# Kernel optimization log

Hardware: AMD Instinct MI355X
Metric: run time of the kernel (lower is better)

## Reference

```python
import jax, jax.numpy as jnp
import numpy as np

B, T, D, H, d = 2, 2048, 1024, 16, 64
INNER = H * d
SCALE = d ** -0.5


def _rope(x, inv_freq):
    # x: [B, H, T, d], interleaved rotary as in the torch module
    t = x.shape[2]
    pos = jnp.arange(t, dtype=jnp.float32)
    freqs = pos[:, None] * inv_freq[None, :]          # [T, d/2]
    cos_f, sin_f = jnp.cos(freqs), jnp.sin(freqs)
    x1, x2 = x[..., 0::2], x[..., 1::2]
    y1 = x1 * cos_f - x2 * sin_f
    y2 = x1 * sin_f + x2 * cos_f
    return jnp.stack([y1, y2], axis=-1).reshape(x.shape)


def setup_inputs() -> dict:
    key = jax.random.key(0)
    ks = jax.random.split(key, 6)
    x = jax.random.normal(ks[0], (B, T, D), jnp.float32)
    W_qkv = jax.random.normal(ks[1], (D, 3 * INNER), jnp.float32) * (D ** -0.5)
    W_out = jax.random.normal(ks[2], (INNER, D), jnp.float32) * (INNER ** -0.5)
    W_dt = jax.random.normal(ks[3], (D, H), jnp.float32) * 0.01
    b_dt = jnp.full((H,), -4.0, jnp.float32)
    W_gsp = jax.random.normal(ks[4], (D, INNER), jnp.float32) * 0.01
    b_gsp = jnp.full((INNER,), -3.0, jnp.float32)
    inv_freq = 1.0 / (10000.0 ** (jnp.arange(0, d, 2, dtype=jnp.float32) / d))
    return {"x": x, "W_qkv": W_qkv, "W_out": W_out, "W_dt": W_dt,
            "b_dt": b_dt, "W_gsp": W_gsp, "b_gsp": b_gsp, "inv_freq": inv_freq}


def reference(x, W_qkv, W_out, W_dt, b_dt, W_gsp, b_gsp, inv_freq):
    qkv = (x @ W_qkv).reshape(B, T, 3, H, d)
    Q = jnp.moveaxis(qkv[:, :, 0], 1, 2)   # [B,H,T,d]
    K = jnp.moveaxis(qkv[:, :, 1], 1, 2)
    V = jnp.moveaxis(qkv[:, :, 2], 1, 2)
    Q = _rope(Q, inv_freq)
    K = _rope(K, inv_freq)

    dt = jax.nn.softplus(x @ W_dt + b_dt)             # [B,T,H]
    gamma = jnp.moveaxis(jnp.exp(-dt), 1, 2)          # [B,H,T]

    p = jax.nn.sigmoid(x @ W_gsp + b_gsp).reshape(B, T, H, d)
    p = jnp.moveaxis(p, 1, 2)                          # [B,H,T,d]
    gamma_eff = gamma[..., None] * (1.0 - p) + p
    gamma_scalar = gamma_eff.mean(axis=-1)            # [B,H,T]
    V = V * (1.0 - p)

    log_gamma = jnp.log(jnp.clip(gamma_scalar, 1e-6, 1.0 - 1e-6))
    lgc = jnp.cumsum(log_gamma, axis=-1)              # [B,H,T]
    log_D = jnp.clip(lgc[..., :, None] - lgc[..., None, :], -20.0, 0.0)
    causal = jnp.tril(jnp.ones((T, T), jnp.float32))
    Dm = jnp.exp(log_D) * causal                      # [B,H,T,T]

    Wscore = jnp.einsum('bhtd,bhsd->bhts', Q * SCALE, K)
    A = Wscore * Dm
    Y = jnp.einsum('bhts,bhsd->bhtd', A, V)
    Y = jnp.moveaxis(Y, 1, 2).reshape(B, T, INNER)
    return Y @ W_out
```

## Files before the change

### kernel.cpp

```cpp
#include <hip/hip_runtime.h>
#include <hip/hip_bf16.h>
#include <math.h>

#define B_     2
#define T_     2048
#define D_     1024
#define H_     16
#define INNER_ 1024
#define NC_    4096
#define SCALE_ 0.125f

typedef unsigned short u16;
typedef short short8 __attribute__((ext_vector_type(8)));
typedef float f32x4 __attribute__((ext_vector_type(4)));
typedef float f32x16 __attribute__((ext_vector_type(16)));
typedef unsigned short u16x4 __attribute__((ext_vector_type(4)));
typedef unsigned int u32x2 __attribute__((ext_vector_type(2)));

__device__ __forceinline__ u16 f2bf(float x) {
  union { float f; unsigned u; } v; v.f = x;
  unsigned r = v.u + 0x7fffu + ((v.u >> 16) & 1u);
  return (u16)(r >> 16);
}
__device__ __forceinline__ float b2f(u16 x) {
  union { unsigned u; float f; } v; v.u = ((unsigned)x) << 16;
  return v.f;
}
__device__ __forceinline__ unsigned cvtpk(float lo, float hi) {
  unsigned r;
  asm("v_cvt_pk_bf16_f32 %0, %1, %2" : "=v"(r) : "v"(lo), "v"(hi));
  return r;
}
__device__ __forceinline__ void gload16(const void* g, void* l) {
  __builtin_amdgcn_global_load_lds(
      (const __attribute__((address_space(1))) void*)g,
      (__attribute__((address_space(3))) void*)l, 16, 0, 0);
}

__global__ __launch_bounds__(256) void prep_kernel(
    const float* __restrict__ x, const float* __restrict__ W_qkv,
    const float* __restrict__ W_gsp, const float* __restrict__ W_out,
    const float* __restrict__ W_dt, const float* __restrict__ inv_freq,
    u16* __restrict__ xb, u16* __restrict__ Wcombt, u16* __restrict__ Woutt,
    u16* __restrict__ Wdtb, float2* __restrict__ tab) {
  const int bid = blockIdx.x, tid = threadIdx.x;
  if (bid < 1280) {
    const float* src; u16* dst; int N, nx, ky;
    if (bid < 768)       { src = W_qkv; dst = Wcombt;                N = 3072; nx = bid % 48;          ky = bid / 48; }
    else if (bid < 1024) { src = W_gsp; dst = Wcombt + 3072 * 1024;  N = 1024; nx = (bid - 768) % 16;  ky = (bid - 768) / 16; }
    else                 { src = W_out; dst = Woutt;                 N = 1024; nx = (bid - 1024) % 16; ky = (bid - 1024) / 16; }
    __shared__ float tile[64][65];
    const int k0 = ky * 64, n0 = nx * 64;
    for (int e = tid; e < 4096; e += 256) {
      int kk = e >> 6, nn = e & 63;
      tile[kk][nn] = src[(size_t)(k0 + kk) * N + n0 + nn];
    }
    __syncthreads();
    for (int e = tid; e < 4096; e += 256) {
      int nn = e >> 6, kk = e & 63;
      dst[(size_t)(n0 + nn) * 1024 + k0 + kk] = f2bf(tile[kk][nn]);
    }
  } else if (bid < 1344) {
    int i = (bid - 1280) * 256 + tid;
    int k = i >> 4, h = i & 15;
    Wdtb[(size_t)h * D_ + k] = f2bf(W_dt[i]);
  } else if (bid < 1600) {
    int i = (bid - 1344) * 256 + tid;
    int t = i >> 5, j = i & 31;
    float s, c;
    sincosf((float)t * inv_freq[j], &s, &c);
    tab[i] = make_float2(c, s);
  } else {
    int base = (bid - 1600) * 1024 + tid;
#pragma unroll
    for (int r = 0; r < 4; ++r) {
      int i = base + r * 256;
      float4 v = *reinterpret_cast<const float4*>(x + (size_t)i * 4);
      u16x4 o; o.x = f2bf(v.x); o.y = f2bf(v.y); o.z = f2bf(v.z); o.w = f2bf(v.w);
      *reinterpret_cast<u16x4*>(xb + (size_t)i * 4) = o;
    }
  }
}

__global__ __launch_bounds__(256) void gamma_kernel(
    const u16* __restrict__ xb, const u16* __restrict__ Wdtb,
    const float* __restrict__ b_dt, float* __restrict__ gam) {
  const int row = blockIdx.x * 4 + (threadIdx.x >> 6);
  const int l = threadIdx.x & 63;
  const int h = l >> 2;
  const int kc = (l & 3) * 256;
  const short8* xp = (const short8*)(xb + (size_t)row * D_ + kc);
  const short8* wp = (const short8*)(Wdtb + h * D_ + kc);
  float s = 0.f;
#pragma unroll
  for (int i = 0; i < 32; ++i) {
    short8 xv = xp[i], wv = wp[i];
#pragma unroll
    for (int j = 0; j < 8; ++j) s += b2f((u16)xv[j]) * b2f((u16)wv[j]);
  }
  s += __shfl_xor(s, 1);
  s += __shfl_xor(s, 2);
  if ((l & 3) == 0) {
    float v = s + b_dt[h];
    float sp = (v > 20.f) ? v : log1pf(__expf(v));
    gam[row * H_ + h] = __expf(-sp);
  }
}

#define SWZG(r) ((((r) & 3) ^ (((r) >> 2) & 1)))

__device__ __forceinline__ void stage_op(const u16* __restrict__ gbase, int kt,
                                         char* ldst, int h, int tid) {
  int r = h * 128 + (tid >> 2);
  int kg = (tid & 3) ^ SWZG(r);
  gload16(gbase + (size_t)r * D_ + kt * 32 + kg * 8,
          ldst + (h * 128 + (tid >> 6) * 16) * 64);
}
__device__ __forceinline__ short8 ldfrag(const char* tile, int row, int g4) {
  return *(const short8*)(tile + row * 64 + ((g4 ^ SWZG(row)) << 4));
}

__global__ __launch_bounds__(512, 2) void gemm_big(
    const u16* __restrict__ A, const u16* __restrict__ Bt,
    u16* __restrict__ C) {
  __shared__ char lds[4 * 32768];
  const int tid = threadIdx.x;
  const int w = tid >> 6, l = tid & 63;
  const int bid = blockIdx.x;
  const int xcd = bid & 7, idx = bid >> 3;
  const int brow = (xcd >> 1) * 4 + (idx & 3);
  const int bcol = (xcd & 1) * 8 + (idx >> 2);
  const int m0 = brow * 256, n0 = bcol * 256;
  const int wr = (w >> 2) * 128, wc = (w & 3) * 64;
  const int ql = l & 15, g4 = l >> 4;

  const u16* Ag = A + (size_t)m0 * D_;
  const u16* Bg = Bt + (size_t)n0 * D_;

  f32x4 acc[8][4] = {};

#pragma unroll
  for (int t = 0; t < 3; ++t) {
    char* bufA = lds + t * 32768;
    char* bufB = bufA + 16384;
    stage_op(Ag, t, bufA, 0, tid); stage_op(Ag, t, bufA, 1, tid);
    stage_op(Bg, t, bufB, 0, tid); stage_op(Bg, t, bufB, 1, tid);
  }

  const int NT = D_ / 32;
  for (int kt = 0; kt < NT; ++kt) {
    if (kt < NT - 2)       asm volatile("s_waitcnt vmcnt(8)" ::: "memory");
    else if (kt == NT - 2) asm volatile("s_waitcnt vmcnt(4)" ::: "memory");
    else                   asm volatile("s_waitcnt vmcnt(0)" ::: "memory");
    __builtin_amdgcn_sched_barrier(0);
    __builtin_amdgcn_s_barrier();
    __builtin_amdgcn_sched_barrier(0);

    char* bufA = lds + (kt & 3) * 32768;
    char* bufB = bufA + 16384;
    char* nbufA = lds + ((kt + 3) & 3) * 32768;
    char* nbufB = nbufA + 16384;
    const bool pre = (kt + 3 < NT);

    if (pre) {
      stage_op(Ag, kt + 3, nbufA, 0, tid);
      stage_op(Ag, kt + 3, nbufA, 1, tid);
    }
    short8 bf[4];
#pragma unroll
    for (int nf = 0; nf < 4; ++nf) bf[nf] = ldfrag(bufB, wc + nf * 16 + ql, g4);
    short8 af[4];
#pragma unroll
    for (int mf = 0; mf < 4; ++mf) af[mf] = ldfrag(bufA, wr + mf * 16 + ql, g4);
    asm volatile("s_waitcnt lgkmcnt(0)" ::: "memory");
    __builtin_amdgcn_sched_barrier(0);
    __builtin_amdgcn_s_setprio(1);
#pragma unroll
    for (int mf = 0; mf < 4; ++mf)
#pragma unroll
      for (int nf = 0; nf < 4; ++nf)
        acc[mf][nf] = __builtin_amdgcn_mfma_f32_16x16x32_bf16(af[mf], bf[nf], acc[mf][nf], 0, 0, 0);
    __builtin_amdgcn_s_setprio(0);
    __builtin_amdgcn_s_barrier();

    if (pre) {
      stage_op(Bg, kt + 3, nbufB, 0, tid);
      stage_op(Bg, kt + 3, nbufB, 1, tid);
    }
    short8 af2[4];
#pragma unroll
    for (int mf = 0; mf < 4; ++mf) af2[mf] = ldfrag(bufA, wr + 64 + mf * 16 + ql, g4);
    asm volatile("s_waitcnt lgkmcnt(0)" ::: "memory");
    __builtin_amdgcn_sched_barrier(0);
    __builtin_amdgcn_s_setprio(1);
#pragma unroll
    for (int mf = 0; mf < 4; ++mf)
#pragma unroll
      for (int nf = 0; nf < 4; ++nf)
        acc[mf + 4][nf] = __builtin_amdgcn_mfma_f32_16x16x32_bf16(af2[mf], bf[nf], acc[mf + 4][nf], 0, 0, 0);
    __builtin_amdgcn_s_setprio(0);
  }

#pragma unroll
  for (int mf = 0; mf < 8; ++mf) {
#pragma unroll
    for (int r = 0; r < 4; ++r) {
      size_t row = (size_t)(m0 + wr + mf * 16 + g4 * 4 + r);
      size_t base = row * NC_ + n0 + wc + ql;
#pragma unroll
      for (int nf = 0; nf < 4; ++nf)
        C[base + nf * 16] = f2bf(acc[mf][nf][r]);
    }
  }
}

template <bool BF16OUT>
__global__ __launch_bounds__(256) void gemm_bt(
    const u16* __restrict__ A, const u16* __restrict__ Bt,
    void* __restrict__ Cv, int M, int N, int K) {
  __shared__ u16 As[2][128 * 64] __attribute__((aligned(16)));
  __shared__ u16 Bs[2][128 * 64] __attribute__((aligned(16)));
  const int tid = threadIdx.x, w = tid >> 6, l = tid & 63;
  const int rpx = (M >> 7) >> 3;
  const int bid = blockIdx.x;
  const int xcd = bid & 7, idx = bid >> 3;
  const int brow = xcd * rpx + (idx % rpx);
  const int bcol = idx / rpx;
  const int m0 = brow * 128, n0 = bcol * 128;
  const int wr = (w >> 1) * 64, wc = (w & 1) * 64;
  const int srow = l >> 3;
  const int kgrp = ((l & 7) ^ srow) * 8;

  f32x4 acc[4][4] = {};

  auto stage = [&](int kt, int bs) {
#pragma unroll
    for (int i = 0; i < 4; ++i) {
      int c = w * 4 + i;
      int row = c * 8 + srow;
      gload16(A + (size_t)(m0 + row) * K + kt * 64 + kgrp, (char*)As[bs] + c * 1024);
      gload16(Bt + (size_t)(n0 + row) * K + kt * 64 + kgrp, (char*)Bs[bs] + c * 1024);
    }
  };

  stage(0, 0);
  const int NT = K >> 6;
  for (int kt = 0; kt < NT; ++kt) {
    if (kt + 1 < NT) {
      stage(kt + 1, (kt + 1) & 1);
      asm volatile("s_waitcnt vmcnt(8)" ::: "memory");
    } else {
      asm volatile("s_waitcnt vmcnt(0)" ::: "memory");
    }
    __builtin_amdgcn_sched_barrier(0);
    __builtin_amdgcn_s_barrier();
    __builtin_amdgcn_sched_barrier(0);
    const char* Asb = (const char*)As[kt & 1];
    const char* Bsb = (const char*)Bs[kt & 1];
#pragma unroll
    for (int kk = 0; kk < 2; ++kk) {
      short8 af[4], bf[4];
#pragma unroll
      for (int i = 0; i < 4; ++i) {
        int ra = wr + i * 16 + (l & 15);
        int sa = kk * 4 + (l >> 4);
        af[i] = *(const short8*)(Asb + ra * 128 + ((sa ^ (ra & 7)) << 4));
        int rb = wc + i * 16 + (l & 15);
        bf[i] = *(const short8*)(Bsb + rb * 128 + ((sa ^ (rb & 7)) << 4));
      }
#pragma unroll
      for (int i = 0; i < 4; ++i)
#pragma unroll
        for (int j = 0; j < 4; ++j)
          acc[i][j] = __builtin_amdgcn_mfma_f32_16x16x32_bf16(af[i], bf[j], acc[i][j], 0, 0, 0);
    }
    if (kt + 1 < NT) __builtin_amdgcn_s_barrier();
  }
#pragma unroll
  for (int i = 0; i < 4; ++i) {
#pragma unroll
    for (int r = 0; r < 4; ++r) {
      size_t row = (size_t)(m0 + wr + i * 16 + (l >> 4) * 4 + r);
      size_t base = row * N + n0 + wc + (l & 15);
#pragma unroll
      for (int j = 0; j < 4; ++j) {
        if (BF16OUT) ((u16*)Cv)[base + j * 16] = f2bf(acc[i][j][r]);
        else         ((float*)Cv)[base + j * 16] = acc[i][j][r];
      }
    }
  }
}

__global__ __launch_bounds__(256) void pointwise_kernel(
    const u16* __restrict__ C, const float* __restrict__ gam,
    const float* __restrict__ b_gsp, const float2* __restrict__ tab,
    u16* __restrict__ Qb, u16* __restrict__ Kb, u16* __restrict__ Vb,
    float* __restrict__ lg) {
  const int row = blockIdx.x * 4 + (threadIdx.x >> 6);
  const int l = threadIdx.x & 63;
  const int b = row >> 11, t = row & (T_ - 1);
  const int h = l >> 2;
  const int dd0 = (l & 3) * 16;
  const int col = h * 64 + dd0;
  const size_t cb = (size_t)row * NC_;

  const float gh = gam[row * H_ + h];
  const short8* qp = (const short8*)(C + cb + col);
  const short8* kp = (const short8*)(C + cb + 1024 + col);
  const short8* vp = (const short8*)(C + cb + 2048 + col);
  const short8* pp = (const short8*)(C + cb + 3072 + col);
  short8 q0 = qp[0], q1 = qp[1];
  short8 k0 = kp[0], k1 = kp[1];
  short8 v0 = vp[0], v1 = vp[1];
  short8 pr0 = pp[0], pr1 = pp[1];

  float ge = 0.f;
  short8 vo0, vo1;
#pragma unroll
  for (int i = 0; i < 8; ++i) {
    float pv = b2f((u16)pr0[i]) + b_gsp[col + i];
    float p = 1.f / (1.f + __expf(-pv));
    ge += gh * (1.f - p) + p;
    vo0[i] = (short)f2bf(b2f((u16)v0[i]) * (1.f - p));
    float pv1 = b2f((u16)pr1[i]) + b_gsp[col + 8 + i];
    float p1 = 1.f / (1.f + __expf(-pv1));
    ge += gh * (1.f - p1) + p1;
    vo1[i] = (short)f2bf(b2f((u16)v1[i]) * (1.f - p1));
  }
  const size_t hm = (((size_t)(b * H_ + h)) * T_ + t) * 64 + dd0;
  ((short8*)(Vb + hm))[0] = vo0;
  ((short8*)(Vb + hm))[1] = vo1;

  ge += __shfl_xor(ge, 1);
  ge += __shfl_xor(ge, 2);
  if ((l & 3) == 0) {
    float gs = ge * (1.f / 64.f);
    gs = fminf(fmaxf(gs, 1e-6f), 1.f - 1e-6f);
    lg[((size_t)(b * H_ + h)) * T_ + t] = logf(gs);
  }

  short8 qo0, qo1, ko0, ko1;
  const float2* cs = tab + t * 32 + (dd0 >> 1);
#pragma unroll
  for (int m = 0; m < 4; ++m) {
    float2 c0 = cs[m];
    float qa = b2f((u16)q0[2 * m]), qb = b2f((u16)q0[2 * m + 1]);
    qo0[2 * m]     = (short)f2bf((qa * c0.x - qb * c0.y) * SCALE_);
    qo0[2 * m + 1] = (short)f2bf((qa * c0.y + qb * c0.x) * SCALE_);
    float ka = b2f((u16)k0[2 * m]), kb = b2f((u16)k0[2 * m + 1]);
    ko0[2 * m]     = (short)f2bf(ka * c0.x - kb * c0.y);
    ko0[2 * m + 1] = (short)f2bf(ka * c0.y + kb * c0.x);
    float2 c1 = cs[4 + m];
    float qa1 = b2f((u16)q1[2 * m]), qb1 = b2f((u16)q1[2 * m + 1]);
    qo1[2 * m]     = (short)f2bf((qa1 * c1.x - qb1 * c1.y) * SCALE_);
    qo1[2 * m + 1] = (short)f2bf((qa1 * c1.y + qb1 * c1.x) * SCALE_);
    float ka1 = b2f((u16)k1[2 * m]), kb1 = b2f((u16)k1[2 * m + 1]);
    ko1[2 * m]     = (short)f2bf(ka1 * c1.x - kb1 * c1.y);
    ko1[2 * m + 1] = (short)f2bf(ka1 * c1.y + kb1 * c1.x);
  }
  ((short8*)(Qb + hm))[0] = qo0; ((short8*)(Qb + hm))[1] = qo1;
  ((short8*)(Kb + hm))[0] = ko0; ((short8*)(Kb + hm))[1] = ko1;
}

__global__ __launch_bounds__(256) void scan_kernel(
    const float* __restrict__ lg, float* __restrict__ lgc) {
  const size_t base = (size_t)blockIdx.x * T_;
  const int tid = threadIdx.x;
  __shared__ float sums[256];
  float loc[8];
  float run = 0.f;
#pragma unroll
  for (int i = 0; i < 8; ++i) { run += lg[base + tid * 8 + i]; loc[i] = run; }
  sums[tid] = run;
  __syncthreads();
  if (tid == 0) {
    float r = 0.f;
    for (int i = 0; i < 256; ++i) { float v = sums[i]; sums[i] = r; r += v; }
  }
  __syncthreads();
  const float off = sums[tid];
#pragma unroll
  for (int i = 0; i < 8; ++i) lgc[base + tid * 8 + i] = off + loc[i];
}

__global__ __launch_bounds__(256) void kv_prep_kernel(
    const u16* __restrict__ Vb, const float* __restrict__ lgc,
    u16* __restrict__ Vtg) {
  const int stile = blockIdx.x;
  const int bh = blockIdx.y;
  const int tid = threadIdx.x;
  __shared__ u16 vt[64][72];
  const size_t base = ((size_t)bh * T_ + (size_t)stile * 64) * 64;
  const float* lgp = lgc + (size_t)bh * T_;
  const float lgb = lgp[stile * 64];
#pragma unroll
  for (int i = 0; i < 2; ++i) {
    int c = tid * 2 + i;
    int row = c >> 3, k8 = (c & 7) * 8;
    float beta = __expf(lgb - lgp[stile * 64 + row]);
    short8 vv = *(const short8*)(Vb + base + row * 64 + k8);
#pragma unroll
    for (int j = 0; j < 8; ++j) vt[row][k8 + j] = f2bf(b2f((u16)vv[j]) * beta);
  }
  __syncthreads();
#pragma unroll
  for (int i = 0; i < 2; ++i) {
    int c = tid * 2 + i;
    int dd = c >> 3, t8 = (c & 7) * 8;
    short8 o;
#pragma unroll
    for (int j = 0; j < 8; ++j) o[j] = (short)vt[t8 + j][dd];
    *(short8*)(Vtg + ((size_t)(bh * 32 + stile) * 64 + dd) * 64 + t8) = o;
  }
}

__global__ __launch_bounds__(256) void attn_mfma(
    const u16* __restrict__ Qb, const u16* __restrict__ Kb,
    const u16* __restrict__ Vtg, const float* __restrict__ lgc,
    u16* __restrict__ Y) {
  const int i = blockIdx.x;
  const int xcd = i & 7;
  const int half = i >> 8;
  const int r = (i >> 3) & 31;
  const int q8 = r >> 2;
  const int bh_hi = r & 3;
  const int qb = half ? (15 - q8) : q8;
  const int bh = xcd + (bh_hi << 3);
  const int b = bh >> 4, h = bh & 15;
  const int tid = threadIdx.x, w = tid >> 6, l = tid & 63;
  const int l31 = l & 31, hi = l >> 5;
  __shared__ u16 Ks[3][64 * 64] __attribute__((aligned(16)));
  __shared__ u16 Vs[3][64 * 64] __attribute__((aligned(16)));
  __shared__ u16 Ps[4][2048] __attribute__((aligned(16)));
  const u16* Qg = Qb + (size_t)bh * T_ * 64;
  const u16* Kg = Kb + (size_t)bh * T_ * 64;
  const u16* Vg = Vtg + (size_t)bh * 32 * 4096;
  const float* lgp = lgc + (size_t)bh * T_;
  const int srow = l >> 3, slot8 = l & 7;

  const int q0 = qb * 128 + w * 32;
  const int qg = q0 + l31;
  short8 qf[4];
#pragma unroll
  for (int kk = 0; kk < 4; ++kk)
    qf[kk] = *(const short8*)(Qg + (size_t)qg * 64 + kk * 16 + hi * 8);
  const float lgq = lgp[qg];
  const float lgtop = lgp[qb * 128];

  char* Pw = (char*)Ps[w];
  const int psw = l31 & 7;

  f32x16 yacc0 = {}, yacc1 = {};

  const int st0 = qb * 2 + 1;
  int s_min;
  {
    int lo = 0, hic = st0;
    while (lo < hic) {
      int mid = (lo + hic) >> 1;
      if (lgtop - lgp[mid * 64 + 63] > -20.f) hic = mid; else lo = mid + 1;
    }
    s_min = lo;
  }

  auto STAGE = [&](int s) {
    const int bs = s % 3;
#pragma unroll
    for (int i2 = 0; i2 < 2; ++i2) {
      int c = w * 2 + i2, row = c * 8 + srow;
      int kg = (slot8 ^ (row & 7)) * 8;
      gload16(Kg + (size_t)(s * 64 + row) * 64 + kg, (char*)Ks[bs] + c * 1024);
      gload16(Vg + (size_t)s * 4096 + row * 64 + kg, (char*)Vs[bs] + c * 1024);
    }
  };

  STAGE(st0);
  if (st0 - 1 >= s_min) STAGE(st0 - 1);

  for (int st = st0; st >= s_min; --st) {
    __builtin_amdgcn_s_barrier();
    if (st - 2 >= s_min) {
      STAGE(st - 2);
      asm volatile("s_waitcnt vmcnt(8)" ::: "memory");
    } else if (st - 1 >= s_min) {
      asm volatile("s_waitcnt vmcnt(4)" ::: "memory");
    } else {
      asm volatile("s_waitcnt vmcnt(0)" ::: "memory");
    }
    __builtin_amdgcn_sched_barrier(0);

    const bool allinv = (st * 64 > q0 + 31);
    if (!allinv) {
      const int bs = st % 3;
      const char* Ksb = (const char*)Ks[bs];
      const char* Vsb = (const char*)Vs[bs];
      const float alpha = __expf(lgq - lgp[st * 64]);
      const bool domask = (st * 64 + 63 > q0);
      const int qrel = qg - st * 64;
#pragma unroll
      for (int sblk = 0; sblk < 2; ++sblk) {
        f32x16 c = {};
        __builtin_amdgcn_s_setprio(1);
#pragma unroll
        for (int kk = 0; kk < 4; ++kk) {
          int row = sblk * 32 + l31;
          short8 kf = *(const short8*)(Ksb + row * 128 + (((kk * 2 + hi) ^ (row & 7)) << 4));
          c = __builtin_amdgcn_mfma_f32_32x32x16_bf16(kf, qf[kk], c, 0, 0, 0);
        }
        __builtin_amdgcn_s_setprio(0);
        if (domask) {
#pragma unroll
          for (int bq = 0; bq < 4; ++bq) {
            float p0 = c[bq * 4 + 0] * alpha, p1 = c[bq * 4 + 1] * alpha;
            float p2 = c[bq * 4 + 2] * alpha, p3 = c[bq * 4 + 3] * alpha;
            int s64 = sblk * 32 + bq * 8 + hi * 4;
            if (s64 + 0 > qrel) p0 = 0.f;
            if (s64 + 1 > qrel) p1 = 0.f;
            if (s64 + 2 > qrel) p2 = 0.f;
            if (s64 + 3 > qrel) p3 = 0.f;
            u32x2 pk; pk.x = cvtpk(p0, p1); pk.y = cvtpk(p2, p3);
            int slot = sblk * 4 + bq;
            *(u32x2*)(Pw + l31 * 128 + ((slot ^ psw) << 4) + hi * 8) = pk;
          }
        } else {
#pragma unroll
          for (int bq = 0; bq < 4; ++bq) {
            u32x2 pk;
            pk.x = cvtpk(c[bq * 4 + 0] * alpha, c[bq * 4 + 1] * alpha);
            pk.y = cvtpk(c[bq * 4 + 2] * alpha, c[bq * 4 + 3] * alpha);
            int slot = sblk * 4 + bq;
            *(u32x2*)(Pw + l31 * 128 + ((slot ^ psw) << 4) + hi * 8) = pk;
          }
        }
      }
#pragma unroll
      for (int kk = 0; kk < 4; ++kk) {
        short8 pf = *(const short8*)(Pw + l31 * 128 + (((kk * 2 + hi) ^ psw) << 4));
        short8 vf0 = *(const short8*)(Vsb + l31 * 128 + (((kk * 2 + hi) ^ (l31 & 7)) << 4));
        short8 vf1 = *(const short8*)(Vsb + (32 + l31) * 128 + (((kk * 2 + hi) ^ (l31 & 7)) << 4));
        __builtin_amdgcn_s_setprio(1);
        yacc0 = __builtin_amdgcn_mfma_f32_32x32x16_bf16(pf, vf0, yacc0, 0, 0, 0);
        yacc1 = __builtin_amdgcn_mfma_f32_32x32x16_bf16(pf, vf1, yacc1, 0, 0, 0);
        __builtin_amdgcn_s_setprio(0);
      }
    }
  }

#pragma unroll
  for (int reg = 0; reg < 16; ++reg) {
    int qrow = (reg & 3) + 8 * (reg >> 2) + 4 * hi;
    size_t rowg = (size_t)(b * T_) + qb * 128 + w * 32 + qrow;
    Y[rowg * INNER_ + h * 64 + l31] = f2bf(yacc0[reg]);
    Y[rowg * INNER_ + h * 64 + 32 + l31] = f2bf(yacc1[reg]);
  }
}

extern "C" void kernel_launch(void* const* d_in, const int* in_sizes, int n_in,
                              void* d_out, int out_size, void* d_ws, size_t ws_size,
                              hipStream_t stream) {
  const float* x        = (const float*)d_in[0];
  const float* W_qkv    = (const float*)d_in[1];
  const float* W_out    = (const float*)d_in[2];
  const float* W_dt     = (const float*)d_in[3];
  const float* b_dt     = (const float*)d_in[4];
  const float* W_gsp    = (const float*)d_in[5];
  const float* b_gsp    = (const float*)d_in[6];
  const float* inv_freq = (const float*)d_in[7];
  float* out = (float*)d_out;

  const int M = B_ * T_;
  char* p = (char*)d_ws;
  auto alloc = [&](size_t bytes) {
    char* r = p; p += (bytes + 255) & ~(size_t)255; return r;
  };
  u16*    xb    = (u16*)alloc((size_t)M * D_ * 2);
  u16*    Wcombt= (u16*)alloc((size_t)NC_ * D_ * 2);
  u16*    Woutt = (u16*)alloc((size_t)D_ * INNER_ * 2);
  u16*    Wdtb  = (u16*)alloc((size_t)H_ * D_ * 2);
  u16*    Cqkvp = (u16*)alloc((size_t)M * NC_ * 2);
  u16*    Qb    = (u16*)alloc((size_t)B_ * H_ * T_ * 64 * 2);
  u16*    Kb    = (u16*)alloc((size_t)B_ * H_ * T_ * 64 * 2);
  u16*    Vb    = (u16*)alloc((size_t)B_ * H_ * T_ * 64 * 2);
  float*  gam   = (float*)alloc((size_t)M * H_ * 4);
  float*  lg    = (float*)alloc((size_t)B_ * H_ * T_ * 4);
  float*  lgc   = (float*)alloc((size_t)B_ * H_ * T_ * 4);
  float2* tab   = (float2*)alloc((size_t)T_ * 32 * 8);
  u16*    Vtg   = Cqkvp;
  u16*    Yb    = Cqkvp + (size_t)4 * 1024 * 1024;

  prep_kernel<<<2624, 256, 0, stream>>>(x, W_qkv, W_gsp, W_out, W_dt, inv_freq,
                                        xb, Wcombt, Woutt, Wdtb, tab);
  gamma_kernel<<<M / 4, 256, 0, stream>>>(xb, Wdtb, b_dt, gam);
  gemm_big<<<256, 512, 0, stream>>>(xb, Wcombt, Cqkvp);

  pointwise_kernel<<<M / 4, 256, 0, stream>>>(Cqkvp, gam, b_gsp, tab,
                                              Qb, Kb, Vb, lg);
  scan_kernel<<<B_ * H_, 256, 0, stream>>>(lg, lgc);
  kv_prep_kernel<<<dim3(T_ / 64, B_ * H_), 256, 0, stream>>>(Vb, lgc, Vtg);

  attn_mfma<<<512, 256, 0, stream>>>(Qb, Kb, Vtg, lgc, Yb);

  gemm_bt<false><<<256, 256, 0, stream>>>(Yb, Woutt, out, M, D_, INNER_);
}
```

Before: 153.8 us.

## Fuse gamma projection into pointwise kernel and shrink big GEMM to 128x256 tiles

Removes the separate gamma kernel and computes the dt projection, softplus and exp inside the pointwise kernel, which saves one launch and the gamma buffer round trip. The large QKV+gate GEMM also changes from 512-thread 256x256 tiles with a 4-stage LDS ring to 256-thread 128x256 tiles with double buffering and a simpler swizzle, launching 512 blocks. This trades pipeline depth and per-block reuse for more blocks and less LDS, and it makes the pointwise kernel do extra dot-product work per row.

```diff
diff --git a/kernel.cpp b/kernel.cpp
--- a/kernel.cpp
+++ b/kernel.cpp
@@ -82,98 +82,64 @@
   }
 }
 
-__global__ __launch_bounds__(256) void gamma_kernel(
-    const u16* __restrict__ xb, const u16* __restrict__ Wdtb,
-    const float* __restrict__ b_dt, float* __restrict__ gam) {
-  const int row = blockIdx.x * 4 + (threadIdx.x >> 6);
-  const int l = threadIdx.x & 63;
-  const int h = l >> 2;
-  const int kc = (l & 3) * 256;
-  const short8* xp = (const short8*)(xb + (size_t)row * D_ + kc);
-  const short8* wp = (const short8*)(Wdtb + h * D_ + kc);
-  float s = 0.f;
-#pragma unroll
-  for (int i = 0; i < 32; ++i) {
-    short8 xv = xp[i], wv = wp[i];
-#pragma unroll
-    for (int j = 0; j < 8; ++j) s += b2f((u16)xv[j]) * b2f((u16)wv[j]);
-  }
-  s += __shfl_xor(s, 1);
-  s += __shfl_xor(s, 2);
-  if ((l & 3) == 0) {
-    float v = s + b_dt[h];
-    float sp = (v > 20.f) ? v : log1pf(__expf(v));
-    gam[row * H_ + h] = __expf(-sp);
-  }
-}
-
-#define SWZG(r) ((((r) & 3) ^ (((r) >> 2) & 1)))
-
-__device__ __forceinline__ void stage_op(const u16* __restrict__ gbase, int kt,
-                                         char* ldst, int h, int tid) {
-  int r = h * 128 + (tid >> 2);
-  int kg = (tid & 3) ^ SWZG(r);
-  gload16(gbase + (size_t)r * D_ + kt * 32 + kg * 8,
-          ldst + (h * 128 + (tid >> 6) * 16) * 64);
-}
-__device__ __forceinline__ short8 ldfrag(const char* tile, int row, int g4) {
-  return *(const short8*)(tile + row * 64 + ((g4 ^ SWZG(row)) << 4));
-}
-
-__global__ __launch_bounds__(512, 2) void gemm_big(
+__global__ __launch_bounds__(256, 2) void gemm_big(
     const u16* __restrict__ A, const u16* __restrict__ Bt,
     u16* __restrict__ C) {
-  __shared__ char lds[4 * 32768];
+  __shared__ u16 As[2][128 * 32] __attribute__((aligned(16)));
+  __shared__ u16 Bs[2][256 * 32] __attribute__((aligned(16)));
   const int tid = threadIdx.x;
   const int w = tid >> 6, l = tid & 63;
   const int bid = blockIdx.x;
   const int xcd = bid & 7, idx = bid >> 3;
-  const int brow = (xcd >> 1) * 4 + (idx & 3);
-  const int bcol = (xcd & 1) * 8 + (idx >> 2);
-  const int m0 = brow * 256, n0 = bcol * 256;
-  const int wr = (w >> 2) * 128, wc = (w & 3) * 64;
+  const int brow = xcd * 4 + (idx & 3);
+  const int bcol = idx >> 2;
+  const int m0 = brow * 128, n0 = bcol * 256;
   const int ql = l & 15, g4 = l >> 4;
+  const int srow = tid >> 2;
+  const int ssl  = (tid & 3) ^ (srow & 3);
 
   const u16* Ag = A + (size_t)m0 * D_;
   const u16* Bg = Bt + (size_t)n0 * D_;
 
+  auto STAGE = [&](int kt, int bp) {
+#pragma unroll
+    for (int c = 0; c < 2; ++c)
+      gload16(Ag + (size_t)(c * 64 + srow) * D_ + kt * 32 + ssl * 8,
+              (char*)As[bp] + c * 4096 + tid * 16);
+#pragma unroll
+    for (int c = 0; c < 4; ++c)
+      gload16(Bg + (size_t)(c * 64 + srow) * D_ + kt * 32 + ssl * 8,
+              (char*)Bs[bp] + c * 4096 + tid * 16);
+  };
+
   f32x4 acc[8][4] = {};
-
-#pragma unroll
-  for (int t = 0; t < 3; ++t) {
-    char* bufA = lds + t * 32768;
-    char* bufB = bufA + 16384;
-    stage_op(Ag, t, bufA, 0, tid); stage_op(Ag, t, bufA, 1, tid);
-    stage_op(Bg, t, bufB, 0, tid); stage_op(Bg, t, bufB, 1, tid);
-  }
+  STAGE(0, 0);
 
   const int NT = D_ / 32;
   for (int kt = 0; kt < NT; ++kt) {
-    if (kt < NT - 2)       asm volatile("s_waitcnt vmcnt(8)" ::: "memory");
-    else if (kt == NT - 2) asm volatile("s_waitcnt vmcnt(4)" ::: "memory");
-    else                   asm volatile("s_waitcnt vmcnt(0)" ::: "memory");
+    const int bp = kt & 1;
+    __builtin_amdgcn_s_barrier();
+    if (kt + 1 < NT) {
+      STAGE(kt + 1, bp ^ 1);
+      asm volatile("s_waitcnt vmcnt(6)" ::: "memory");
+    } else {
+      asm volatile("s_waitcnt vmcnt(0)" ::: "memory");
+    }
     __builtin_amdgcn_sched_barrier(0);
-    __builtin_amdgcn_s_barrier();
-    __builtin_amdgcn_sched_barrier(0);
-
-    char* bufA = lds + (kt & 3) * 32768;
-    char* bufB = bufA + 16384;
-    char* nbufA = lds + ((kt + 3) & 3) * 32768;
-    char* nbufB = nbufA + 16384;
-    const bool pre = (kt + 3 < NT);
-
-    if (pre) {
-      stage_op(Ag, kt + 3, nbufA, 0, tid);
-      stage_op(Ag, kt + 3, nbufA, 1, tid);
-    }
-    short8 bf[4];
-#pragma unroll
-    for (int nf = 0; nf < 4; ++nf) bf[nf] = ldfrag(bufB, wc + nf * 16 + ql, g4);
-    short8 af[4];
-#pragma unroll
-    for (int mf = 0; mf < 4; ++mf) af[mf] = ldfrag(bufA, wr + mf * 16 + ql, g4);
-    asm volatile("s_waitcnt lgkmcnt(0)" ::: "memory");
-    __builtin_amdgcn_sched_barrier(0);
+
+    const char* Asb = (const char*)As[bp];
+    const char* Bsb = (const char*)Bs[bp];
+    short8 bf[4], af[4];
+#pragma unroll
+    for (int nf = 0; nf < 4; ++nf) {
+      int row = w * 64 + nf * 16 + ql;
+      bf[nf] = *(const short8*)(Bsb + row * 64 + ((g4 ^ (row & 3)) << 4));
+    }
+#pragma unroll
+    for (int mf = 0; mf < 4; ++mf) {
+      int row = mf * 16 + ql;
+      af[mf] = *(const short8*)(Asb + row * 64 + ((g4 ^ (row & 3)) << 4));
+    }
     __builtin_amdgcn_s_setprio(1);
 #pragma unroll
     for (int mf = 0; mf < 4; ++mf)
@@ -181,23 +147,17 @@
       for (int nf = 0; nf < 4; ++nf)
         acc[mf][nf] = __builtin_amdgcn_mfma_f32_16x16x32_bf16(af[mf], bf[nf], acc[mf][nf], 0, 0, 0);
     __builtin_amdgcn_s_setprio(0);
-    __builtin_amdgcn_s_barrier();
-
-    if (pre) {
-      stage_op(Bg, kt + 3, nbufB, 0, tid);
-      stage_op(Bg, kt + 3, nbufB, 1, tid);
-    }
-    short8 af2[4];
-#pragma unroll
-    for (int mf = 0; mf < 4; ++mf) af2[mf] = ldfrag(bufA, wr + 64 + mf * 16 + ql, g4);
-    asm volatile("s_waitcnt lgkmcnt(0)" ::: "memory");
-    __builtin_amdgcn_sched_barrier(0);
+#pragma unroll
+    for (int mf = 0; mf < 4; ++mf) {
+      int row = 64 + mf * 16 + ql;
+      af[mf] = *(const short8*)(Asb + row * 64 + ((g4 ^ (row & 3)) << 4));
+    }
     __builtin_amdgcn_s_setprio(1);
 #pragma unroll
     for (int mf = 0; mf < 4; ++mf)
 #pragma unroll
       for (int nf = 0; nf < 4; ++nf)
-        acc[mf + 4][nf] = __builtin_amdgcn_mfma_f32_16x16x32_bf16(af2[mf], bf[nf], acc[mf + 4][nf], 0, 0, 0);
+        acc[mf + 4][nf] = __builtin_amdgcn_mfma_f32_16x16x32_bf16(af[mf], bf[nf], acc[mf + 4][nf], 0, 0, 0);
     __builtin_amdgcn_s_setprio(0);
   }
 
@@ -205,8 +165,8 @@
   for (int mf = 0; mf < 8; ++mf) {
 #pragma unroll
     for (int r = 0; r < 4; ++r) {
-      size_t row = (size_t)(m0 + wr + mf * 16 + g4 * 4 + r);
-      size_t base = row * NC_ + n0 + wc + ql;
+      size_t row = (size_t)(m0 + mf * 16 + g4 * 4 + r);
+      size_t base = row * NC_ + n0 + w * 64 + ql;
 #pragma unroll
       for (int nf = 0; nf < 4; ++nf)
         C[base + nf * 16] = f2bf(acc[mf][nf][r]);
@@ -292,7 +252,8 @@
 }
 
 __global__ __launch_bounds__(256) void pointwise_kernel(
-    const u16* __restrict__ C, const float* __restrict__ gam,
+    const u16* __restrict__ C, const u16* __restrict__ xb,
+    const u16* __restrict__ Wdtb, const float* __restrict__ b_dt,
     const float* __restrict__ b_gsp, const float2* __restrict__ tab,
     u16* __restrict__ Qb, u16* __restrict__ Kb, u16* __restrict__ Vb,
     float* __restrict__ lg) {
@@ -304,7 +265,24 @@
   const int col = h * 64 + dd0;
   const size_t cb = (size_t)row * NC_;
 
-  const float gh = gam[row * H_ + h];
+  float gsum = 0.f;
+  {
+    const int kc = (l & 3) * 256;
+    const short8* xpg = (const short8*)(xb + (size_t)row * D_ + kc);
+    const short8* wpg = (const short8*)(Wdtb + h * D_ + kc);
+#pragma unroll
+    for (int i = 0; i < 32; ++i) {
+      short8 xv = xpg[i], wv = wpg[i];
+#pragma unroll
+      for (int j = 0; j < 8; ++j) gsum += b2f((u16)xv[j]) * b2f((u16)wv[j]);
+    }
+    gsum += __shfl_xor(gsum, 1);
+    gsum += __shfl_xor(gsum, 2);
+  }
+  const float dtv = gsum + b_dt[h];
+  const float sp = (dtv > 20.f) ? dtv : log1pf(__expf(dtv));
+  const float gh = __expf(-sp);
+
   const short8* qp = (const short8*)(C + cb + col);
   const short8* kp = (const short8*)(C + cb + 1024 + col);
   const short8* vp = (const short8*)(C + cb + 2048 + col);
@@ -581,7 +559,6 @@
   u16*    Qb    = (u16*)alloc((size_t)B_ * H_ * T_ * 64 * 2);
   u16*    Kb    = (u16*)alloc((size_t)B_ * H_ * T_ * 64 * 2);
   u16*    Vb    = (u16*)alloc((size_t)B_ * H_ * T_ * 64 * 2);
-  float*  gam   = (float*)alloc((size_t)M * H_ * 4);
   float*  lg    = (float*)alloc((size_t)B_ * H_ * T_ * 4);
   float*  lgc   = (float*)alloc((size_t)B_ * H_ * T_ * 4);
   float2* tab   = (float2*)alloc((size_t)T_ * 32 * 8);
@@ -590,11 +567,10 @@
 
   prep_kernel<<<2624, 256, 0, stream>>>(x, W_qkv, W_gsp, W_out, W_dt, inv_freq,
                                         xb, Wcombt, Woutt, Wdtb, tab);
-  gamma_kernel<<<M / 4, 256, 0, stream>>>(xb, Wdtb, b_dt, gam);
-  gemm_big<<<256, 512, 0, stream>>>(xb, Wcombt, Cqkvp);
-
-  pointwise_kernel<<<M / 4, 256, 0, stream>>>(Cqkvp, gam, b_gsp, tab,
-                                              Qb, Kb, Vb, lg);
+  gemm_big<<<512, 256, 0, stream>>>(xb, Wcombt, Cqkvp);
+
+  pointwise_kernel<<<M / 4, 256, 0, stream>>>(Cqkvp, xb, Wdtb, b_dt, b_gsp,
+                                              tab, Qb, Kb, Vb, lg);
   scan_kernel<<<B_ * H_, 256, 0, stream>>>(lg, lgc);
   kv_prep_kernel<<<dim3(T_ / 64, B_ * H_), 256, 0, stream>>>(Vb, lgc, Vtg);
 
```

Measured after the change: 148.7 us. 3.3% less time.
